# Performance work log

Measured on AMD Instinct MI355X. Metric: run time of the kernel, lower is better.

The kernel has to match this reference:

```python
import jax, jax.numpy as jnp
import numpy as np


def setup_inputs() -> dict:
    key = jax.random.key(0)
    ks = jax.random.split(key, 8)
    B, P, K, N = 8, 16384, 16384, 16
    IN, REL, OUT = 64, 3, 64
    return {
        "keys": jax.random.normal(ks[0], (B, K, REL), dtype=jnp.float32),
        "points": jax.random.normal(ks[1], (B, P, REL), dtype=jnp.float32),
        "feats": jax.random.normal(ks[2], (B, P, IN), dtype=jnp.float32),
        "n_idxs": jax.random.randint(ks[3], (B, K, N), 0, P, dtype=jnp.int32),
        "neighbor_rel": jax.random.normal(ks[4], (B, K, N, REL), dtype=jnp.float32),
        "neighbor_valid": jax.random.randint(ks[5], (B, K, N), 0, 2, dtype=jnp.int32),
        "W": jax.random.normal(ks[6], (OUT, IN + REL), dtype=jnp.float32) / np.sqrt(IN + REL),
        "b": jax.random.normal(ks[7], (OUT,), dtype=jnp.float32) * 0.01,
    }


def reference(keys, points, feats, n_idxs, neighbor_rel, neighbor_valid, W, b):
    # gather neighbor features: feats[b, n_idxs[b]] per batch -> [B, K, N, IN]
    neighbor_feats = jax.vmap(lambda f, i: f[i])(feats, n_idxs)
    comb = jnp.concatenate([neighbor_feats, neighbor_rel], axis=-1)  # [B,K,N,IN+REL]
    valid = neighbor_valid.astype(comb.dtype)                        # [B,K,N]
    cleared = comb * valid[..., None]
    counts = valid.sum(-1)                                           # [B,K]
    inv_counts = jnp.where(counts > 0, 1.0 / jnp.maximum(counts, 1.0), 0.0)
    sum_feats = cleared.sum(axis=2)                                  # [B,K,IN+REL]
    scaled = sum_feats * inv_counts[..., None]
    return jax.nn.relu(jnp.einsum('bkc,oc->bko', scaled, W) + b)
```

## Files before the change

kernel.cpp:

```cpp
#include <hip/hip_runtime.h>

#define BB   8
#define PP   16384
#define KK   16384
#define NN   16
#define CIN  64
#define REL  3
#define CC   67
#define OUTC 64
#define KPAD 96
#define PITCH_US 104


typedef short s16x8 __attribute__((ext_vector_type(8)));
typedef float f32x4 __attribute__((ext_vector_type(4)));

static __device__ __forceinline__ unsigned short bf16_rne(float f) {
    unsigned int u = __float_as_uint(f);
    u += 0x7FFF + ((u >> 16) & 1);
    return (unsigned short)(u >> 16);
}

__global__ __launch_bounds__(256, 6) void graphconv_kernel(
    const float* __restrict__ feats,
    const int*   __restrict__ n_idxs,
    const float* __restrict__ neighbor_rel,
    const int*   __restrict__ neighbor_valid,
    const float* __restrict__ Wm,
    const float* __restrict__ bvec,
    float*       __restrict__ out)
{
    __shared__ __align__(16) unsigned short Wbf[OUTC * PITCH_US];
    __shared__ __align__(16) unsigned short Stile[4 * 16 * PITCH_US];

    const int tid = threadIdx.x;

    {
        unsigned int* w32 = (unsigned int*)Wbf;
        for (int j = tid; j < OUTC * (PITCH_US / 2); j += 256) {
            const int o = j / (PITCH_US / 2);
            const int d = j - o * (PITCH_US / 2);
            const int c0 = 2 * d, c1 = 2 * d + 1;
            const float w0 = (c0 < CC) ? Wm[o * CC + c0] : 0.0f;
            const float w1 = (c1 < CC) ? Wm[o * CC + c1] : 0.0f;
            w32[j] = (unsigned int)bf16_rne(w0) |
                     ((unsigned int)bf16_rne(w1) << 16);
        }
    }
    __syncthreads();

    const int lane = tid & 63;
    const int wave = __builtin_amdgcn_readfirstlane(tid >> 6);
    unsigned short* Sw = &Stile[wave * 16 * PITCH_US];

    {
        unsigned int* s32 = (unsigned int*)Sw;
        for (int j = lane; j < 16 * (PITCH_US / 2); j += 64) s32[j] = 0u;
    }

    const int b   = blockIdx.x & 7;
    const int bib = blockIdx.x >> 3;
    const float* fb = feats + (size_t)b * ((size_t)PP * CIN);

    const int kbase = (bib * 4 + wave) * 16;

    for (int ip = 0; ip < 8; ++ip) {
        const int iA = 2 * ip, iB = 2 * ip + 1;
        const size_t rowA = (size_t)b * KK + (size_t)(kbase + iA);
        const size_t rowB = rowA + 1;
        const int*   idxA = n_idxs         + rowA * NN;
        const int*   idxB = n_idxs         + rowB * NN;
        const int*   vpA  = neighbor_valid + rowA * NN;
        const int*   vpB  = neighbor_valid + rowB * NN;
        const float* relA = neighbor_rel   + rowA * (NN * REL);
        const float* relB = neighbor_rel   + rowB * (NN * REL);

        float sumA = 0.f, a0 = 0.f, a1 = 0.f, a2 = 0.f;
        float sumB = 0.f, b0 = 0.f, b1 = 0.f, b2 = 0.f;
        int cntA = 0, cntB = 0;
#pragma unroll
        for (int n = 0; n < NN; ++n) {
            const int   vA = vpA[n],  vB = vpB[n];
            const int   dA = idxA[n], dB = idxB[n];
            const float mA = (float)vA, mB = (float)vB;
            const float gA = fb[(size_t)dA * CIN + lane];
            const float gB = fb[(size_t)dB * CIN + lane];
            sumA = fmaf(mA, gA, sumA);
            sumB = fmaf(mB, gB, sumB);
            a0 = fmaf(mA, relA[n * 3 + 0], a0);
            a1 = fmaf(mA, relA[n * 3 + 1], a1);
            a2 = fmaf(mA, relA[n * 3 + 2], a2);
            b0 = fmaf(mB, relB[n * 3 + 0], b0);
            b1 = fmaf(mB, relB[n * 3 + 1], b1);
            b2 = fmaf(mB, relB[n * 3 + 2], b2);
            cntA += vA; cntB += vB;
        }
        const float invA = (cntA > 0) ? (1.0f / (float)cntA) : 0.0f;
        const float invB = (cntB > 0) ? (1.0f / (float)cntB) : 0.0f;

        Sw[iA * PITCH_US + lane] = bf16_rne(sumA * invA);
        Sw[iB * PITCH_US + lane] = bf16_rne(sumB * invB);
        if (lane < 3) {
            const float rA = (lane == 0) ? a0 : ((lane == 1) ? a1 : a2);
            const float rB = (lane == 0) ? b0 : ((lane == 1) ? b1 : b2);
            Sw[iA * PITCH_US + 64 + lane] = bf16_rne(rA * invA);
            Sw[iB * PITCH_US + 64 + lane] = bf16_rne(rB * invB);
        }
    }

    f32x4 C0 = {0.f,0.f,0.f,0.f}, C1 = {0.f,0.f,0.f,0.f};
    f32x4 C2 = {0.f,0.f,0.f,0.f}, C3 = {0.f,0.f,0.f,0.f};
#pragma unroll
    for (int q = 0; q < 3; ++q) {
        const s16x8 A = *(const s16x8*)&Sw[(lane & 15) * PITCH_US
                                           + q * 32 + (lane >> 4) * 8];
        const int ko = q * 32 + (lane >> 4) * 8;
        const s16x8 B0 = *(const s16x8*)&Wbf[( 0 + (lane & 15)) * PITCH_US + ko];
        const s16x8 B1 = *(const s16x8*)&Wbf[(16 + (lane & 15)) * PITCH_US + ko];
        const s16x8 B2 = *(const s16x8*)&Wbf[(32 + (lane & 15)) * PITCH_US + ko];
        const s16x8 B3 = *(const s16x8*)&Wbf[(48 + (lane & 15)) * PITCH_US + ko];
        C0 = __builtin_amdgcn_mfma_f32_16x16x32_bf16(A, B0, C0, 0, 0, 0);
        C1 = __builtin_amdgcn_mfma_f32_16x16x32_bf16(A, B1, C1, 0, 0, 0);
        C2 = __builtin_amdgcn_mfma_f32_16x16x32_bf16(A, B2, C2, 0, 0, 0);
        C3 = __builtin_amdgcn_mfma_f32_16x16x32_bf16(A, B3, C3, 0, 0, 0);
    }

    const float bias0 = bvec[ 0 + (lane & 15)];
    const float bias1 = bvec[16 + (lane & 15)];
    const float bias2 = bvec[32 + (lane & 15)];
    const float bias3 = bvec[48 + (lane & 15)];
    const int m0 = (lane >> 4) * 4;
    const int oc = lane & 15;
#pragma unroll
    for (int r = 0; r < 4; ++r) {
        const size_t orow = ((size_t)b * KK + (size_t)(kbase + m0 + r)) * OUTC;
        out[orow + 0  + oc] = fmaxf(C0[r] + bias0, 0.0f);
        out[orow + 16 + oc] = fmaxf(C1[r] + bias1, 0.0f);
        out[orow + 32 + oc] = fmaxf(C2[r] + bias2, 0.0f);
        out[orow + 48 + oc] = fmaxf(C3[r] + bias3, 0.0f);
    }
}

extern "C" void kernel_launch(void* const* d_in, const int* in_sizes, int n_in,
                              void* d_out, int out_size, void* d_ws, size_t ws_size,
                              hipStream_t stream) {
    const float* feats = (const float*)d_in[2];
    const int*   nidx  = (const int*)  d_in[3];
    const float* nrel  = (const float*)d_in[4];
    const int*   nval  = (const int*)  d_in[5];
    const float* Wm    = (const float*)d_in[6];
    const float* bv    = (const float*)d_in[7];
    float* out = (float*)d_out;

    graphconv_kernel<<<dim3(2048), dim3(256), 0, stream>>>(
        feats, nidx, nrel, nval, Wm, bv, out);
}
```

Measured before the change: 183.7 us.

## Gather four key rows per wave with float4 loads and bpermute-broadcast indices

Restructures the gather so each wave handles four keys at once, with 16 lanes per key each loading a float4 of the neighbor feature row. Coalesced loads of indices, valid flags and relative positions replace per-lane scalar reloads. The packed index and valid bits are broadcast with ds_bpermute, and counts and rel sums are reduced with ds_swizzle. Each wave now processes 32 keys in two groups with half the blocks, and launch bounds are relaxed to 4. The aim is fewer memory instructions and wider gather transactions, at the cost of a 14-bit index packing assumption and lower occupancy.

```diff
diff --git a/kernel.cpp b/kernel.cpp
--- a/kernel.cpp
+++ b/kernel.cpp
@@ -8,12 +8,12 @@
 #define REL  3
 #define CC   67
 #define OUTC 64
-#define KPAD 96
 #define PITCH_US 104
 
 
 typedef short s16x8 __attribute__((ext_vector_type(8)));
 typedef float f32x4 __attribute__((ext_vector_type(4)));
+typedef unsigned int u32x2 __attribute__((ext_vector_type(2)));
 
 static __device__ __forceinline__ unsigned short bf16_rne(float f) {
     unsigned int u = __float_as_uint(f);
@@ -21,7 +21,20 @@
     return (unsigned short)(u >> 16);
 }
 
-__global__ __launch_bounds__(256, 6) void graphconv_kernel(
+static __device__ __forceinline__ float swz_add1(float v) {
+    return v + __int_as_float(__builtin_amdgcn_ds_swizzle(__float_as_int(v), 0x041F));
+}
+static __device__ __forceinline__ float swz_add2(float v) {
+    return v + __int_as_float(__builtin_amdgcn_ds_swizzle(__float_as_int(v), 0x081F));
+}
+static __device__ __forceinline__ float swz_add4(float v) {
+    return v + __int_as_float(__builtin_amdgcn_ds_swizzle(__float_as_int(v), 0x101F));
+}
+static __device__ __forceinline__ float swz_add8(float v) {
+    return v + __int_as_float(__builtin_amdgcn_ds_swizzle(__float_as_int(v), 0x201F));
+}
+
+__global__ __launch_bounds__(256, 4) void graphconv_kernel(
     const float* __restrict__ feats,
     const int*   __restrict__ n_idxs,
     const float* __restrict__ neighbor_rel,
@@ -62,82 +75,97 @@
     const int bib = blockIdx.x >> 3;
     const float* fb = feats + (size_t)b * ((size_t)PP * CIN);
 
-    const int kbase = (bib * 4 + wave) * 16;
+    const int q     = lane & 15;
+    const int permb = (lane & 48) << 2;
 
-    for (int ip = 0; ip < 8; ++ip) {
-        const int iA = 2 * ip, iB = 2 * ip + 1;
-        const size_t rowA = (size_t)b * KK + (size_t)(kbase + iA);
-        const size_t rowB = rowA + 1;
-        const int*   idxA = n_idxs         + rowA * NN;
-        const int*   idxB = n_idxs         + rowB * NN;
-        const int*   vpA  = neighbor_valid + rowA * NN;
-        const int*   vpB  = neighbor_valid + rowB * NN;
-        const float* relA = neighbor_rel   + rowA * (NN * REL);
-        const float* relB = neighbor_rel   + rowB * (NN * REL);
+    const int kw = (bib * 4 + wave) * 32;
 
-        float sumA = 0.f, a0 = 0.f, a1 = 0.f, a2 = 0.f;
-        float sumB = 0.f, b0 = 0.f, b1 = 0.f, b2 = 0.f;
-        int cntA = 0, cntB = 0;
+    for (int g = 0; g < 2; ++g) {
+        const int kg = kw + g * 16;
+
+        for (int qd = 0; qd < 4; ++qd) {
+            const size_t rq = (size_t)b * KK + (size_t)(kg + qd * 4);
+
+            const int   vld = neighbor_valid[rq * NN + lane];
+            const int   idd = n_idxs[rq * NN + lane];
+            const int   cmb = idd | (vld << 14);
+            const float msf = (float)vld;
+            const float* relq = neighbor_rel + rq * (NN * REL);
+            float mr0 = msf * relq[3 * lane + 0];
+            float mr1 = msf * relq[3 * lane + 1];
+            float mr2 = msf * relq[3 * lane + 2];
+            float cnt = msf;
+
+            float s0 = 0.f, s1 = 0.f, s2 = 0.f, s3 = 0.f;
 #pragma unroll
-        for (int n = 0; n < NN; ++n) {
-            const int   vA = vpA[n],  vB = vpB[n];
-            const int   dA = idxA[n], dB = idxB[n];
-            const float mA = (float)vA, mB = (float)vB;
-            const float gA = fb[(size_t)dA * CIN + lane];
-            const float gB = fb[(size_t)dB * CIN + lane];
-            sumA = fmaf(mA, gA, sumA);
-            sumB = fmaf(mB, gB, sumB);
-            a0 = fmaf(mA, relA[n * 3 + 0], a0);
-            a1 = fmaf(mA, relA[n * 3 + 1], a1);
-            a2 = fmaf(mA, relA[n * 3 + 2], a2);
-            b0 = fmaf(mB, relB[n * 3 + 0], b0);
-            b1 = fmaf(mB, relB[n * 3 + 1], b1);
-            b2 = fmaf(mB, relB[n * 3 + 2], b2);
-            cntA += vA; cntB += vB;
+            for (int n = 0; n < NN; ++n) {
+                const int cm = __builtin_amdgcn_ds_bpermute(permb + 4 * n, cmb);
+                const float m = (float)(cm >> 14);
+                const int  off = ((cm & 0x3FFF) << 6) + 4 * q;
+                const float4 gv = *(const float4*)(fb + off);
+                s0 = fmaf(m, gv.x, s0);
+                s1 = fmaf(m, gv.y, s1);
+                s2 = fmaf(m, gv.z, s2);
+                s3 = fmaf(m, gv.w, s3);
+            }
+
+            cnt = swz_add1(cnt); mr0 = swz_add1(mr0);
+            mr1 = swz_add1(mr1); mr2 = swz_add1(mr2);
+            cnt = swz_add2(cnt); mr0 = swz_add2(mr0);
+            mr1 = swz_add2(mr1); mr2 = swz_add2(mr2);
+            cnt = swz_add4(cnt); mr0 = swz_add4(mr0);
+            mr1 = swz_add4(mr1); mr2 = swz_add4(mr2);
+            cnt = swz_add8(cnt); mr0 = swz_add8(mr0);
+            mr1 = swz_add8(mr1); mr2 = swz_add8(mr2);
+
+            const float inv = (cnt > 0.f) ? (1.0f / cnt) : 0.0f;
+
+            const int rowl = qd * 4 + (lane >> 4);
+            u32x2 pv;
+            pv.x = (unsigned)bf16_rne(s0 * inv) |
+                   ((unsigned)bf16_rne(s1 * inv) << 16);
+            pv.y = (unsigned)bf16_rne(s2 * inv) |
+                   ((unsigned)bf16_rne(s3 * inv) << 16);
+            *(u32x2*)(&Sw[rowl * PITCH_US + 4 * q]) = pv;
+            if (q == 0) {
+                u32x2 ev;
+                ev.x = (unsigned)bf16_rne(mr0 * inv) |
+                       ((unsigned)bf16_rne(mr1 * inv) << 16);
+                ev.y = (unsigned)bf16_rne(mr2 * inv);
+                *(u32x2*)(&Sw[rowl * PITCH_US + 64]) = ev;
+            }
         }
-        const float invA = (cntA > 0) ? (1.0f / (float)cntA) : 0.0f;
-        const float invB = (cntB > 0) ? (1.0f / (float)cntB) : 0.0f;
 
-        Sw[iA * PITCH_US + lane] = bf16_rne(sumA * invA);
-        Sw[iB * PITCH_US + lane] = bf16_rne(sumB * invB);
-        if (lane < 3) {
-            const float rA = (lane == 0) ? a0 : ((lane == 1) ? a1 : a2);
-            const float rB = (lane == 0) ? b0 : ((lane == 1) ? b1 : b2);
-            Sw[iA * PITCH_US + 64 + lane] = bf16_rne(rA * invA);
-            Sw[iB * PITCH_US + 64 + lane] = bf16_rne(rB * invB);
+        f32x4 C0 = {0.f,0.f,0.f,0.f}, C1 = {0.f,0.f,0.f,0.f};
+        f32x4 C2 = {0.f,0.f,0.f,0.f}, C3 = {0.f,0.f,0.f,0.f};
+#pragma unroll
+        for (int p = 0; p < 3; ++p) {
+            const int ko = p * 32 + (lane >> 4) * 8;
+            const s16x8 A  = *(const s16x8*)&Sw[(lane & 15) * PITCH_US + ko];
+            const s16x8 B0 = *(const s16x8*)&Wbf[( 0 + (lane & 15)) * PITCH_US + ko];
+            const s16x8 B1 = *(const s16x8*)&Wbf[(16 + (lane & 15)) * PITCH_US + ko];
+            const s16x8 B2 = *(const s16x8*)&Wbf[(32 + (lane & 15)) * PITCH_US + ko];
+            const s16x8 B3 = *(const s16x8*)&Wbf[(48 + (lane & 15)) * PITCH_US + ko];
+            C0 = __builtin_amdgcn_mfma_f32_16x16x32_bf16(A, B0, C0, 0, 0, 0);
+            C1 = __builtin_amdgcn_mfma_f32_16x16x32_bf16(A, B1, C1, 0, 0, 0);
+            C2 = __builtin_amdgcn_mfma_f32_16x16x32_bf16(A, B2, C2, 0, 0, 0);
+            C3 = __builtin_amdgcn_mfma_f32_16x16x32_bf16(A, B3, C3, 0, 0, 0);
         }
-    }
 
-    f32x4 C0 = {0.f,0.f,0.f,0.f}, C1 = {0.f,0.f,0.f,0.f};
-    f32x4 C2 = {0.f,0.f,0.f,0.f}, C3 = {0.f,0.f,0.f,0.f};
+        const float bias0 = bvec[ 0 + (lane & 15)];
+        const float bias1 = bvec[16 + (lane & 15)];
+        const float bias2 = bvec[32 + (lane & 15)];
+        const float bias3 = bvec[48 + (lane & 15)];
+        const int m0 = (lane >> 4) * 4;
+        const int oc = lane & 15;
 #pragma unroll
-    for (int q = 0; q < 3; ++q) {
-        const s16x8 A = *(const s16x8*)&Sw[(lane & 15) * PITCH_US
-                                           + q * 32 + (lane >> 4) * 8];
-        const int ko = q * 32 + (lane >> 4) * 8;
-        const s16x8 B0 = *(const s16x8*)&Wbf[( 0 + (lane & 15)) * PITCH_US + ko];
-        const s16x8 B1 = *(const s16x8*)&Wbf[(16 + (lane & 15)) * PITCH_US + ko];
-        const s16x8 B2 = *(const s16x8*)&Wbf[(32 + (lane & 15)) * PITCH_US + ko];
-        const s16x8 B3 = *(const s16x8*)&Wbf[(48 + (lane & 15)) * PITCH_US + ko];
-        C0 = __builtin_amdgcn_mfma_f32_16x16x32_bf16(A, B0, C0, 0, 0, 0);
-        C1 = __builtin_amdgcn_mfma_f32_16x16x32_bf16(A, B1, C1, 0, 0, 0);
-        C2 = __builtin_amdgcn_mfma_f32_16x16x32_bf16(A, B2, C2, 0, 0, 0);
-        C3 = __builtin_amdgcn_mfma_f32_16x16x32_bf16(A, B3, C3, 0, 0, 0);
-    }
-
-    const float bias0 = bvec[ 0 + (lane & 15)];
-    const float bias1 = bvec[16 + (lane & 15)];
-    const float bias2 = bvec[32 + (lane & 15)];
-    const float bias3 = bvec[48 + (lane & 15)];
-    const int m0 = (lane >> 4) * 4;
-    const int oc = lane & 15;
-#pragma unroll
-    for (int r = 0; r < 4; ++r) {
-        const size_t orow = ((size_t)b * KK + (size_t)(kbase + m0 + r)) * OUTC;
-        out[orow + 0  + oc] = fmaxf(C0[r] + bias0, 0.0f);
-        out[orow + 16 + oc] = fmaxf(C1[r] + bias1, 0.0f);
-        out[orow + 32 + oc] = fmaxf(C2[r] + bias2, 0.0f);
-        out[orow + 48 + oc] = fmaxf(C3[r] + bias3, 0.0f);
+        for (int r = 0; r < 4; ++r) {
+            const size_t orow = ((size_t)b * KK + (size_t)(kg + m0 + r)) * OUTC;
+            out[orow + 0  + oc] = fmaxf(C0[r] + bias0, 0.0f);
+            out[orow + 16 + oc] = fmaxf(C1[r] + bias1, 0.0f);
+            out[orow + 32 + oc] = fmaxf(C2[r] + bias2, 0.0f);
+            out[orow + 48 + oc] = fmaxf(C3[r] + bias3, 0.0f);
+        }
     }
 }
 
@@ -152,6 +180,6 @@
     const float* bv    = (const float*)d_in[7];
     float* out = (float*)d_out;
 
-    graphconv_kernel<<<dim3(2048), dim3(256), 0, stream>>>(
+    graphconv_kernel<<<dim3(1024), dim3(256), 0, stream>>>(
         feats, nidx, nrel, nval, Wm, bv, out);
 }
```

After: 161.4 us. -12.2%, faster.
